# Optimization experiments

Measured on AMD Instinct MI355X. Metric: run time of the kernel, lower is better.

Reference implementation:

```python
import jax, jax.numpy as jnp
import numpy as np

LSTM_H = 128
HID = 64
EMB = 64
GRU2_H = 50
B, T = 2048, 200
NODE_NUM = 50000


def _lstm_dir(x_proj, w_hh, reverse):
    # x_proj: (T, B, 4H) = x @ W_ih^T + b_ih + b_hh, precomputed
    Bn = x_proj.shape[1]
    H = w_hh.shape[1]
    h0 = jnp.zeros((Bn, H), x_proj.dtype)

    def step(carry, xp):
        h, c = carry
        gates = xp + h @ w_hh.T
        i, f, g, o = jnp.split(gates, 4, axis=-1)  # torch gate order i,f,g,o
        i = jax.nn.sigmoid(i); f = jax.nn.sigmoid(f)
        g = jnp.tanh(g); o = jax.nn.sigmoid(o)
        c = f * c + i * g
        h = o * jnp.tanh(c)
        return (h, c), h

    (hT, _), hs = jax.lax.scan(step, (h0, h0), x_proj, reverse=reverse)
    return hs, hT  # hs: (T,B,H) time-aligned; hT: final hidden of this direction


def _bilstm(x, wih_f, whh_f, b_f, wih_b, whh_b, b_b):
    # x: (B,T,I) batch_first -> scan over time
    xt = jnp.swapaxes(x, 0, 1)  # (T,B,I)
    hs_f, h_f = _lstm_dir(xt @ wih_f.T + b_f, whh_f, False)
    hs_b, h_b = _lstm_dir(xt @ wih_b.T + b_b, whh_b, True)
    out = jnp.concatenate([hs_f, hs_b], axis=-1)  # (T,B,2H)
    return jnp.swapaxes(out, 0, 1), jnp.stack([h_f, h_b])  # (B,T,2H), (2,B,H)


def _gru(x, h, wih, whh, bih, bhh):
    gi = x @ wih.T + bih
    gh = h @ whh.T + bhh
    ir, iz, inn = jnp.split(gi, 3, axis=-1)  # torch gate order r,z,n
    hr, hz, hn = jnp.split(gh, 3, axis=-1)
    r = jax.nn.sigmoid(ir + hr)
    z = jax.nn.sigmoid(iz + hz)
    n = jnp.tanh(inn + r * hn)
    return (1.0 - z) * n + z * h


def setup_inputs() -> dict:
    key = jax.random.key(0)
    ks = iter(jax.random.split(key, 40))
    s = 0.05
    d = {}
    d['node_data'] = jax.random.randint(next(ks), (B, 2), 0, NODE_NUM)
    d['edge_data'] = jax.random.uniform(next(ks), (B, T, 1), jnp.float32)
    d['emb'] = jax.random.normal(next(ks), (NODE_NUM, EMB), jnp.float32) * s
    # LSTM 1: input 1, hidden 128, bidirectional (b = b_ih + b_hh fused)
    d['l1_wih_f'] = jax.random.normal(next(ks), (4 * LSTM_H, 1), jnp.float32) * s
    d['l1_whh_f'] = jax.random.normal(next(ks), (4 * LSTM_H, LSTM_H), jnp.float32) * s
    d['l1_b_f'] = jax.random.normal(next(ks), (4 * LSTM_H,), jnp.float32) * s
    d['l1_wih_b'] = jax.random.normal(next(ks), (4 * LSTM_H, 1), jnp.float32) * s
    d['l1_whh_b'] = jax.random.normal(next(ks), (4 * LSTM_H, LSTM_H), jnp.float32) * s
    d['l1_b_b'] = jax.random.normal(next(ks), (4 * LSTM_H,), jnp.float32) * s
    # LSTM 2: input 256, hidden 128, bidirectional
    d['l2_wih_f'] = jax.random.normal(next(ks), (4 * LSTM_H, 2 * LSTM_H), jnp.float32) * s
    d['l2_whh_f'] = jax.random.normal(next(ks), (4 * LSTM_H, LSTM_H), jnp.float32) * s
    d['l2_b_f'] = jax.random.normal(next(ks), (4 * LSTM_H,), jnp.float32) * s
    d['l2_wih_b'] = jax.random.normal(next(ks), (4 * LSTM_H, 2 * LSTM_H), jnp.float32) * s
    d['l2_whh_b'] = jax.random.normal(next(ks), (4 * LSTM_H, LSTM_H), jnp.float32) * s
    d['l2_b_b'] = jax.random.normal(next(ks), (4 * LSTM_H,), jnp.float32) * s
    # encoder FCs
    d['fc1_w'] = jax.random.normal(next(ks), (2 * LSTM_H, 2 * LSTM_H), jnp.float32) * s
    d['fc1_b'] = jnp.zeros((2 * LSTM_H,), jnp.float32)
    d['fc2_w'] = jax.random.normal(next(ks), (HID, 2 * LSTM_H), jnp.float32) * s
    d['fc2_b'] = jnp.zeros((HID,), jnp.float32)
    # GRUCell 1: input 1, hidden HID+EMB=128
    G1 = HID + EMB
    d['g1_wih'] = jax.random.normal(next(ks), (3 * G1, 1), jnp.float32) * s
    d['g1_whh'] = jax.random.normal(next(ks), (3 * G1, G1), jnp.float32) * s
    d['g1_bih'] = jax.random.normal(next(ks), (3 * G1,), jnp.float32) * s
    d['g1_bhh'] = jax.random.normal(next(ks), (3 * G1,), jnp.float32) * s
    # GRUCell 2: input 128, hidden 50
    d['g2_wih'] = jax.random.normal(next(ks), (3 * GRU2_H, G1), jnp.float32) * s
    d['g2_whh'] = jax.random.normal(next(ks), (3 * GRU2_H, GRU2_H), jnp.float32) * s
    d['g2_bih'] = jax.random.normal(next(ks), (3 * GRU2_H,), jnp.float32) * s
    d['g2_bhh'] = jax.random.normal(next(ks), (3 * GRU2_H,), jnp.float32) * s
    # decoder FC: 50 -> 1
    d['dec_w'] = jax.random.normal(next(ks), (1, GRU2_H), jnp.float32) * s
    d['dec_b'] = jnp.zeros((1,), jnp.float32)
    return d


def reference(node_data, edge_data, emb,
              l1_wih_f, l1_whh_f, l1_b_f, l1_wih_b, l1_whh_b, l1_b_b,
              l2_wih_f, l2_whh_f, l2_b_f, l2_wih_b, l2_whh_b, l2_b_b,
              fc1_w, fc1_b, fc2_w, fc2_b,
              g1_wih, g1_whh, g1_bih, g1_bhh,
              g2_wih, g2_whh, g2_bih, g2_bhh,
              dec_w, dec_b):
    # ---- encoder ----
    node_embs = emb[node_data]                      # (B,2,EMB)
    node_emb = node_embs.mean(axis=1)               # (head+tail)/2
    h1_out, hn1 = _bilstm(edge_data, l1_wih_f, l1_whh_f, l1_b_f,
                          l1_wih_b, l1_whh_b, l1_b_b)
    _, hn2 = _bilstm(h1_out, l2_wih_f, l2_whh_f, l2_b_f,
                     l2_wih_b, l2_whh_b, l2_b_b)
    # faithful to original: view (2,B,128) -> (-1, 256) row-major (interleaves dir/batch)
    hidden_lstm = hn1.reshape(-1, 2 * LSTM_H) + hn2.reshape(-1, 2 * LSTM_H)
    h_fc1 = jax.nn.sigmoid(hidden_lstm @ fc1_w.T + fc1_b)  # dropout = identity (eval)
    temp_emb = jax.nn.sigmoid(h_fc1 @ fc2_w.T + fc2_b)
    hidden = jnp.concatenate([temp_emb, node_emb], axis=1)  # (B, HID+EMB)
    # ---- decoder: sequential GRU unroll as a scan ----
    Bn, max_len = edge_data.shape[0], edge_data.shape[1]
    h2_0 = jnp.zeros((Bn, GRU2_H), edge_data.dtype)

    def dstep(carry, _):
        res, h1, h2 = carry
        h1n = _gru(res, h1, g1_wih, g1_whh, g1_bih, g1_bhh)
        h2n = _gru(h1n, h2, g2_wih, g2_whh, g2_bih, g2_bhh)
        resn = jax.nn.sigmoid(h2n @ dec_w.T + dec_b)        # (B,1)
        return (resn, h1n, h2n), resn

    init = (edge_data[:, -1], hidden, h2_0)
    _, results = jax.lax.scan(dstep, init, None, length=max_len)
    return jnp.swapaxes(results, 0, 1)  # (B, max_len, 1)
```

## Files before the change

### kernel.cpp

```cpp
#include <hip/hip_runtime.h>
#include <stdint.h>

typedef short bf16x8 __attribute__((ext_vector_type(8)));
typedef float f32x4  __attribute__((ext_vector_type(4)));
typedef unsigned short u16;

#define NBATCH 2048
#define NT 200

#define MFMA_AG(accv, av, wfrag) \
  asm("v_mfma_f32_16x16x32_bf16 %0, %1, %2, %0" : "+v"(accv) : "v"(av), "a"(wfrag))
#define SEED_A(x) asm volatile("" : "+a"(x))

#define OFF_HN1   209715200ull
#define OFF_HN2   211812352ull
#define OFF_ZC    213909504ull

__device__ __forceinline__ short f2bf(float f){
  union { float f; uint32_t u; } v; v.f = f;
  uint32_t u = v.u;
  u += 0x7fffu + ((u >> 16) & 1u);
  return (short)(u >> 16);
}
__device__ __forceinline__ float sigm(float x){
  return __builtin_amdgcn_rcpf(1.0f + __expf(-x));
}
__device__ __forceinline__ float tanh_(float x){
  return fmaf(-2.0f, __builtin_amdgcn_rcpf(1.0f + __expf(2.0f * x)), 1.0f);
}

__global__ void prep_l12(const float* __restrict__ l1hf, const float* __restrict__ l1hb,
                         const float* __restrict__ l2wf, const float* __restrict__ l2hf,
                         const float* __restrict__ l2wb, const float* __restrict__ l2hb,
                         u16* __restrict__ wl1, u16* __restrict__ wl2)
{
  int idx = blockIdx.x * 256 + threadIdx.x;
  if (idx < 16384){
    int tid = idx & 511, r = idx >> 9;
    int kt = r & 3, g = (r >> 2) & 3, d = r >> 4;
    const float* whh = d ? l1hb : l1hf;
    int wv = tid >> 6, ln = tid & 63, lr = ln & 15, lk = ln >> 4;
    int n = g * 128 + wv * 16 + lr;
    const float* s = whh + (size_t)n * 128 + kt * 32 + lk * 8;
    bf16x8 w;
#pragma unroll
    for (int i = 0; i < 8; ++i) w[i] = f2bf(s[i]);
    *(bf16x8*)(wl1 + (size_t)idx * 8) = w;
  } else {
    int j = idx - 16384;
    int tid = j & 511, r = j >> 9;
    int kt = r % 12, rg = r / 12;
    int g = rg & 3, d = rg >> 2;
    const float* wih = d ? l2wb : l2wf;
    const float* whh = d ? l2hb : l2hf;
    int wv = tid >> 6, ln = tid & 63, lr = ln & 15, lk = ln >> 4;
    int n = g * 128 + wv * 16 + lr;
    const float* s = (kt < 8) ? (wih + (size_t)n * 256 + kt * 32 + lk * 8)
                              : (whh + (size_t)n * 128 + (kt - 8) * 32 + lk * 8);
    bf16x8 w;
#pragma unroll
    for (int i = 0; i < 8; ++i) w[i] = f2bf(s[i]);
    *(bf16x8*)(wl2 + (size_t)j * 8) = w;
  }
}

__global__ void prep_dec(const float* __restrict__ g1whh, const float* __restrict__ g2wih,
                         const float* __restrict__ g2whh,
                         u16* __restrict__ wd1, u16* __restrict__ wd2i, u16* __restrict__ wd2h)
{
  int idx = blockIdx.x * 256 + threadIdx.x;
  if (idx < 6144){
    int tid = idx & 511, r = idx >> 9;
    int kt = r & 3, g = r >> 2;
    int wv = tid >> 6, ln = tid & 63, lr = ln & 15, lk = ln >> 4;
    int n = g * 128 + wv * 16 + lr;
    const float* s = g1whh + (size_t)n * 128 + kt * 32 + lk * 8;
    bf16x8 w;
#pragma unroll
    for (int i = 0; i < 8; ++i) w[i] = f2bf(s[i]);
    *(bf16x8*)(wd1 + (size_t)idx * 8) = w;
  } else if (idx < 9216){
    int j = idx - 6144;
    int tid = j & 255, r = j >> 8;
    int kt = r & 3, g = r >> 2;
    int wv = tid >> 6, ln = tid & 63, lr = ln & 15, lk = ln >> 4;
    int jj = wv * 16 + lr;
    bf16x8 w;
#pragma unroll
    for (int i = 0; i < 8; ++i){
      int k = kt * 32 + lk * 8 + i;
      w[i] = (jj < 50) ? f2bf(g2wih[(size_t)(g * 50 + jj) * 128 + k]) : (short)0;
    }
    *(bf16x8*)(wd2i + (size_t)j * 8) = w;
  } else {
    int j = idx - 9216;
    int tid = j & 255, r = j >> 8;
    int kt = r & 1, g = r >> 1;
    int wv = tid >> 6, ln = tid & 63, lr = ln & 15, lk = ln >> 4;
    int jj = wv * 16 + lr;
    bf16x8 w;
#pragma unroll
    for (int i = 0; i < 8; ++i){
      int k = kt * 32 + lk * 8 + i;
      w[i] = (jj < 50 && k < 50) ? f2bf(g2whh[(size_t)(g * 50 + jj) * 50 + k]) : (short)0;
    }
    *(bf16x8*)(wd2h + (size_t)j * 8) = w;
  }
}

__global__ void prep_fcT(const float* __restrict__ fc1w, const float* __restrict__ fc2w,
                         float* __restrict__ fc1wT, float* __restrict__ fc2wT)
{
  int idx = blockIdx.x * 256 + threadIdx.x;
  if (idx < 65536){
    int n = idx & 255, k = idx >> 8;
    fc1wT[(size_t)k * 256 + n] = fc1w[(size_t)n * 256 + k];
  } else {
    int j = idx - 65536;
    int m = j & 63, k = j >> 6;
    fc2wT[(size_t)k * 64 + m] = fc2w[(size_t)m * 256 + k];
  }
}

__global__ void k_node(const int* __restrict__ nd, const float* __restrict__ emb,
                       float* __restrict__ ne){
  int t = blockIdx.x * 256 + threadIdx.x;
  if (t >= NBATCH * 64) return;
  int row = t >> 6, e = t & 63;
  int i0 = nd[row * 2], i1 = nd[row * 2 + 1];
  ne[t] = 0.5f * (emb[(size_t)i0 * 64 + e] + emb[(size_t)i1 * 64 + e]);
}

__global__ __launch_bounds__(512) __attribute__((amdgpu_waves_per_eu(2, 2))) void k_l1(
    const float* __restrict__ edge, const u16* __restrict__ wl1,
    const float* __restrict__ wih_f, const float* __restrict__ b_f,
    const float* __restrict__ wih_b, const float* __restrict__ b_b,
    u16* __restrict__ h1out, float* __restrict__ hn1)
{
  const int bid = blockIdx.x;
  const int dir = bid >> 7;
  const int b0  = (bid & 127) * 16;
  const float* wih = dir ? wih_b : wih_f;
  const float* bia = dir ? b_b  : b_f;

  const int tid = threadIdx.x;
  const int wv  = tid >> 6;
  const int ln  = tid & 63;
  const int lr  = ln & 15;
  const int lk  = ln >> 4;

  __shared__ __align__(16) short hbf[2][16 * 128];
  __shared__ float xall[16][NT];

  bf16x8 W[4][4];
  const u16* wb = wl1 + (size_t)dir * 16 * 512 * 8;
  float wv_[4], bv_[4];
#pragma unroll
  for (int g = 0; g < 4; ++g){
    int n = g * 128 + wv * 16 + lr;
    wv_[g] = wih[n];
    bv_[g] = bia[n];
#pragma unroll
    for (int kt = 0; kt < 4; ++kt){
      W[g][kt] = *(const bf16x8*)(wb + ((size_t)(g * 4 + kt) * 512 + tid) * 8);
      SEED_A(W[g][kt]);
    }
  }
  for (int i = tid; i < 16 * 128; i += 512) hbf[0][i] = 0;
  for (int i = tid; i < 16 * NT; i += 512){
    int r = i / NT, t = i - r * NT;
    xall[r][t] = edge[(b0 + r) * NT + t];
  }
  float cst[4] = {0.f, 0.f, 0.f, 0.f};
  float hseg[4] = {0.f, 0.f, 0.f, 0.f};
  __syncthreads();

  for (int s = 0; s < NT; ++s){
    const int p = s & 1;
    const int t = dir ? (NT - 1 - s) : s;

    const char* hb = (const char*)hbf + p * (16 * 256);
    f32x4 acc[4];
    float xq[4];
#pragma unroll
    for (int q = 0; q < 4; ++q) xq[q] = xall[lk * 4 + q][t];
#pragma unroll
    for (int g = 0; g < 4; ++g){
#pragma unroll
      for (int q = 0; q < 4; ++q) acc[g][q] = fmaf(xq[q], wv_[g], bv_[g]);
    }
#pragma unroll
    for (int kt = 0; kt < 4; ++kt){
      int off = lr * 256 + ((kt * 64 + lk * 16) ^ ((lr & 7) << 4));
      bf16x8 a = *(const bf16x8*)(hb + off);
#pragma unroll
      for (int g = 0; g < 4; ++g) MFMA_AG(acc[g], a, W[g][kt]);
    }
    char* hbw = (char*)hbf + (p ^ 1) * (16 * 256);
#pragma unroll
    for (int q = 0; q < 4; ++q){
      float iv = sigm(acc[0][q]);
      float fv = sigm(acc[1][q]);
      float gv = tanh_(acc[2][q]);
      float ov = sigm(acc[3][q]);
      cst[q] = fv * cst[q] + iv * gv;
      hseg[q] = ov * tanh_(cst[q]);
      short hv = f2bf(hseg[q]);
      int r = lk * 4 + q, j = wv * 16 + lr;
      h1out[((size_t)t * NBATCH + b0 + r) * 256 + dir * 128 + j] = (u16)hv;
      *(short*)(hbw + r * 256 + ((2 * j) ^ ((r & 7) << 4))) = hv;
    }
    __syncthreads();
  }
#pragma unroll
  for (int q = 0; q < 4; ++q)
    hn1[((size_t)dir * NBATCH + b0 + lk * 4 + q) * 128 + wv * 16 + lr] = hseg[q];
}

__global__ __launch_bounds__(512) __attribute__((amdgpu_waves_per_eu(2, 2))) void k_l2(
    const u16* __restrict__ h1out, const u16* __restrict__ wl2,
    const float* __restrict__ b_f, const float* __restrict__ b_b,
    float* __restrict__ hn2)
{
  const int bid = blockIdx.x;
  const int dir = bid >> 7;
  const int b0  = (bid & 127) * 16;
  const float* bia = dir ? b_b : b_f;

  const int tid = threadIdx.x;
  const int wv  = tid >> 6;
  const int ln  = tid & 63;
  const int lr  = ln & 15;
  const int lk  = ln >> 4;

  __shared__ __align__(16) short wlds[16 * 512 * 8];
  __shared__ __align__(16) short Ab[2][16 * 384];

  const u16* wb = wl2 + (size_t)dir * 48 * 512 * 8;
#pragma unroll
  for (int f = 0; f < 16; ++f){
    int g = f >> 2, kt = f & 3;
    *(bf16x8*)&wlds[((size_t)f * 512 + tid) * 8] =
        *(const bf16x8*)(wb + ((size_t)(g * 12 + kt) * 512 + tid) * 8);
  }
  bf16x8 Wa[4][8];
  float bv_[4];
#pragma unroll
  for (int g = 0; g < 4; ++g){
    bv_[g] = bia[g * 128 + wv * 16 + lr];
#pragma unroll
    for (int k8 = 0; k8 < 8; ++k8){
      Wa[g][k8] = *(const bf16x8*)(wb + ((size_t)(g * 12 + 4 + k8) * 512 + tid) * 8);
      SEED_A(Wa[g][k8]);
    }
  }
  for (int i = tid; i < 16 * 128; i += 512){
    int r = i >> 7, j = i & 127;
    *(short*)((char*)Ab + r * 768 + ((512 + 2 * j) ^ ((r & 7) << 4))) = 0;
  }
  const int sr = tid >> 5, sg = tid & 31;
  {
    int t0 = dir ? NT - 1 : 0;
    bf16x8 v = *(const bf16x8*)(h1out + ((size_t)t0 * NBATCH + b0 + sr) * 256 + sg * 8);
    *(bf16x8*)((char*)Ab + sr * 768 + ((sg * 16) ^ ((sr & 7) << 4))) = v;
  }
  float cst[4] = {0.f, 0.f, 0.f, 0.f};
  float hseg[4] = {0.f, 0.f, 0.f, 0.f};
  __syncthreads();

  for (int s = 0; s < NT; ++s){
    const int p = s & 1;
    const int t = dir ? (NT - 1 - s) : s;
    const int tn = dir ? (t > 0 ? t - 1 : 0) : (t < NT - 1 ? t + 1 : NT - 1);
    bf16x8 xr = *(const bf16x8*)(h1out + ((size_t)tn * NBATCH + b0 + sr) * 256 + sg * 8);

    const char* ab = (const char*)Ab + p * (16 * 768);
    f32x4 acc[4];
#pragma unroll
    for (int g = 0; g < 4; ++g){
#pragma unroll
      for (int q = 0; q < 4; ++q) acc[g][q] = bv_[g];
    }
#pragma unroll
    for (int kt = 0; kt < 4; ++kt){
      int off = lr * 768 + ((kt * 64 + lk * 16) ^ ((lr & 7) << 4));
      bf16x8 a = *(const bf16x8*)(ab + off);
#pragma unroll
      for (int g = 0; g < 4; ++g){
        bf16x8 w = *(const bf16x8*)&wlds[((size_t)(g * 4 + kt) * 512 + tid) * 8];
        acc[g] = __builtin_amdgcn_mfma_f32_16x16x32_bf16(a, w, acc[g], 0, 0, 0);
      }
    }
#pragma unroll
    for (int k8 = 0; k8 < 8; ++k8){
      int kt = 4 + k8;
      int off = lr * 768 + ((kt * 64 + lk * 16) ^ ((lr & 7) << 4));
      bf16x8 a = *(const bf16x8*)(ab + off);
#pragma unroll
      for (int g = 0; g < 4; ++g) MFMA_AG(acc[g], a, Wa[g][k8]);
    }
    char* abw = (char*)Ab + (p ^ 1) * (16 * 768);
#pragma unroll
    for (int q = 0; q < 4; ++q){
      float iv = sigm(acc[0][q]);
      float fv = sigm(acc[1][q]);
      float gv = tanh_(acc[2][q]);
      float ov = sigm(acc[3][q]);
      cst[q] = fv * cst[q] + iv * gv;
      hseg[q] = ov * tanh_(cst[q]);
      int r = lk * 4 + q, j = wv * 16 + lr;
      *(short*)(abw + r * 768 + ((512 + 2 * j) ^ ((r & 7) << 4))) = f2bf(hseg[q]);
    }
    *(bf16x8*)(abw + sr * 768 + ((sg * 16) ^ ((sr & 7) << 4))) = xr;
    __syncthreads();
  }
#pragma unroll
  for (int q = 0; q < 4; ++q)
    hn2[((size_t)dir * NBATCH + b0 + lk * 4 + q) * 128 + wv * 16 + lr] = hseg[q];
}

__global__ __launch_bounds__(256) void k_fc(
    const float* __restrict__ hn1, const float* __restrict__ hn2,
    const float* __restrict__ fc1wT, const float* __restrict__ fc1b,
    const float* __restrict__ fc2wT, const float* __restrict__ fc2b,
    const float* __restrict__ ne, float* __restrict__ hidden)
{
  __shared__ float X[16][256];
  __shared__ float Y[16][256];
  const int b0 = blockIdx.x * 16;
  const int tid = threadIdx.x;
  for (int i = tid; i < 16 * 256; i += 256){
    int rr = i >> 8, cc = i & 255;
    size_t o = (size_t)(b0 + rr) * 256 + cc;
    X[rr][cc] = hn1[o] + hn2[o];
  }
  __syncthreads();
  {
    const int n = tid;
    float a[16];
#pragma unroll
    for (int r = 0; r < 16; ++r) a[r] = fc1b[n];
    for (int k = 0; k < 256; ++k){
      float w = fc1wT[(size_t)k * 256 + n];
#pragma unroll
      for (int r = 0; r < 16; ++r) a[r] = fmaf(X[r][k], w, a[r]);
    }
#pragma unroll
    for (int r = 0; r < 16; ++r) Y[r][n] = sigm(a[r]);
  }
  __syncthreads();
  {
    const int m = tid & 63, rg = tid >> 6;
    float a2[4];
#pragma unroll
    for (int q = 0; q < 4; ++q) a2[q] = fc2b[m];
    for (int k = 0; k < 256; ++k){
      float w = fc2wT[(size_t)k * 64 + m];
#pragma unroll
      for (int q = 0; q < 4; ++q) a2[q] = fmaf(Y[rg * 4 + q][k], w, a2[q]);
    }
#pragma unroll
    for (int q = 0; q < 4; ++q)
      hidden[(size_t)(b0 + rg * 4 + q) * 128 + m] = sigm(a2[q]);
  }
  for (int i = tid; i < 16 * 64; i += 256){
    int rr = i >> 6, e = i & 63;
    hidden[(size_t)(b0 + rr) * 128 + 64 + e] = ne[(size_t)(b0 + rr) * 64 + e];
  }
}

__global__ __launch_bounds__(512) __attribute__((amdgpu_waves_per_eu(2, 2))) void k_dec(
    const float* __restrict__ edge, const float* __restrict__ hidden,
    const float* __restrict__ g1wih, const float* __restrict__ g1bih,
    const float* __restrict__ g1bhh, const u16* __restrict__ wd1,
    const float* __restrict__ g2bih, const float* __restrict__ g2bhh,
    const u16* __restrict__ wd2i, const u16* __restrict__ wd2h,
    const float* __restrict__ decw, const float* __restrict__ decb,
    float* __restrict__ out)
{
  const int b0 = blockIdx.x * 16;
  const int tid = threadIdx.x;
  const int wv  = tid >> 6;
  const int ln  = tid & 63;
  const int lr  = ln & 15;
  const int lk  = ln >> 4;

  __shared__ __align__(16) short h1bf[2][16 * 128];
  __shared__ __align__(16) short h2bf[2][16 * 64];
  __shared__ float part[2][4][16];

  bf16x8 W1[3][4];
  float wih1v[3], bih1v[3], bhh1v[3];
#pragma unroll
  for (int g = 0; g < 3; ++g){
    int n = g * 128 + wv * 16 + lr;
    wih1v[g] = g1wih[n];
    bih1v[g] = g1bih[n];
    bhh1v[g] = g1bhh[n];
#pragma unroll
    for (int kt = 0; kt < 4; ++kt){
      W1[g][kt] = *(const bf16x8*)(wd1 + ((size_t)(g * 4 + kt) * 512 + tid) * 8);
      SEED_A(W1[g][kt]);
    }
  }
  bf16x8 Wi2[3][4], Wh2[3][2];
  float bih2v[3] = {0,0,0}, bhh2v[3] = {0,0,0}, dwv = 0.f;
  const int jj = wv * 16 + lr;
  if (wv < 4){
    bool nv_ = (jj < 50);
    dwv = nv_ ? decw[jj] : 0.f;
#pragma unroll
    for (int g = 0; g < 3; ++g){
      bih2v[g] = nv_ ? g2bih[g * 50 + jj] : 0.f;
      bhh2v[g] = nv_ ? g2bhh[g * 50 + jj] : 0.f;
#pragma unroll
      for (int kt = 0; kt < 4; ++kt){
        Wi2[g][kt] = *(const bf16x8*)(wd2i + ((size_t)(g * 4 + kt) * 256 + tid) * 8);
        SEED_A(Wi2[g][kt]);
      }
#pragma unroll
      for (int kt = 0; kt < 2; ++kt){
        Wh2[g][kt] = *(const bf16x8*)(wd2h + ((size_t)(g * 2 + kt) * 256 + tid) * 8);
        SEED_A(Wh2[g][kt]);
      }
    }
  }
  float h1s[4], h2s[4] = {0.f, 0.f, 0.f, 0.f}, e4[4];
#pragma unroll
  for (int q = 0; q < 4; ++q){
    h1s[q] = hidden[(size_t)(b0 + lk * 4 + q) * 128 + wv * 16 + lr];
    int r = lk * 4 + q, j = wv * 16 + lr;
    *(short*)((char*)h1bf + r * 256 + ((2 * j) ^ ((r & 7) << 4))) = f2bf(h1s[q]);
    e4[q] = edge[(b0 + r) * NT + NT - 1];
  }
  for (int i = tid; i < 16 * 64; i += 512) h2bf[0][i] = 0;
  const float db = decb[0];
  __syncthreads();

  for (int s = 0; s < NT; ++s){
    const int p = s & 1;
    float res_q[4];
    if (s == 0){
#pragma unroll
      for (int q = 0; q < 4; ++q) res_q[q] = e4[q];
    } else {
#pragma unroll
      for (int q = 0; q < 4; ++q){
        int row = lk * 4 + q;
        float sum = part[p][0][row] + part[p][1][row] + part[p][2][row] + part[p][3][row] + db;
        res_q[q] = sigm(sum);
        if (wv == 0 && lr == 0) out[(size_t)(b0 + row) * NT + (s - 1)] = res_q[q];
      }
    }
    const char* h1r = (const char*)h1bf + p * (16 * 256);
    f32x4 ar, az, an;
#pragma unroll
    for (int q = 0; q < 4; ++q){ ar[q] = bhh1v[0]; az[q] = bhh1v[1]; an[q] = bhh1v[2]; }
#pragma unroll
    for (int kt = 0; kt < 4; ++kt){
      int off = lr * 256 + ((kt * 64 + lk * 16) ^ ((lr & 7) << 4));
      bf16x8 a = *(const bf16x8*)(h1r + off);
      MFMA_AG(ar, a, W1[0][kt]);
      MFMA_AG(az, a, W1[1][kt]);
      MFMA_AG(an, a, W1[2][kt]);
    }
    char* h1w = (char*)h1bf + (p ^ 1) * (16 * 256);
#pragma unroll
    for (int q = 0; q < 4; ++q){
      float res = res_q[q];
      float rv = sigm(fmaf(res, wih1v[0], bih1v[0]) + ar[q]);
      float zv = sigm(fmaf(res, wih1v[1], bih1v[1]) + az[q]);
      float nv = tanh_(fmaf(res, wih1v[2], bih1v[2]) + rv * an[q]);
      h1s[q] = (1.f - zv) * nv + zv * h1s[q];
      int r = lk * 4 + q, j = wv * 16 + lr;
      *(short*)(h1w + r * 256 + ((2 * j) ^ ((r & 7) << 4))) = f2bf(h1s[q]);
    }
    __syncthreads();
    if (wv < 4){
      f32x4 gi0, gi1, gi2v, gh0, gh1, gh2v;
#pragma unroll
      for (int q = 0; q < 4; ++q){
        gi0[q] = bih2v[0]; gi1[q] = bih2v[1]; gi2v[q] = bih2v[2];
        gh0[q] = bhh2v[0]; gh1[q] = bhh2v[1]; gh2v[q] = bhh2v[2];
      }
      const char* h1n = (const char*)h1bf + (p ^ 1) * (16 * 256);
#pragma unroll
      for (int kt = 0; kt < 4; ++kt){
        int off = lr * 256 + ((kt * 64 + lk * 16) ^ ((lr & 7) << 4));
        bf16x8 a = *(const bf16x8*)(h1n + off);
        MFMA_AG(gi0,  a, Wi2[0][kt]);
        MFMA_AG(gi1,  a, Wi2[1][kt]);
        MFMA_AG(gi2v, a, Wi2[2][kt]);
      }
      const char* h2r = (const char*)h2bf + p * (16 * 128);
#pragma unroll
      for (int kt = 0; kt < 2; ++kt){
        int off = lr * 128 + ((kt * 64 + lk * 16) ^ ((lr & 7) << 4));
        bf16x8 a = *(const bf16x8*)(h2r + off);
        MFMA_AG(gh0,  a, Wh2[0][kt]);
        MFMA_AG(gh1,  a, Wh2[1][kt]);
        MFMA_AG(gh2v, a, Wh2[2][kt]);
      }
      char* h2w = (char*)h2bf + (p ^ 1) * (16 * 128);
      float pd[4];
#pragma unroll
      for (int q = 0; q < 4; ++q){
        float r2 = sigm(gi0[q] + gh0[q]);
        float z2 = sigm(gi1[q] + gh1[q]);
        float n2 = tanh_(gi2v[q] + r2 * gh2v[q]);
        h2s[q] = (1.f - z2) * n2 + z2 * h2s[q];
        pd[q] = h2s[q] * dwv;
        int r = lk * 4 + q, j = wv * 16 + lr;
        *(short*)(h2w + r * 128 + ((2 * j) ^ ((r & 7) << 4))) = f2bf(h2s[q]);
      }
#pragma unroll
      for (int m = 1; m < 16; m <<= 1){
#pragma unroll
        for (int q = 0; q < 4; ++q) pd[q] += __shfl_xor(pd[q], m);
      }
      if (lr == 0){
#pragma unroll
        for (int q = 0; q < 4; ++q) part[p ^ 1][wv][lk * 4 + q] = pd[q];
      }
    }
    __syncthreads();
  }
  if (wv == 0 && lr == 0){
#pragma unroll
    for (int q = 0; q < 4; ++q){
      int row = lk * 4 + q;
      float sum = part[0][0][row] + part[0][1][row] + part[0][2][row] + part[0][3][row] + db;
      out[(size_t)(b0 + row) * NT + (NT - 1)] = sigm(sum);
    }
  }
}

extern "C" void kernel_launch(void* const* d_in, const int* in_sizes, int n_in,
                              void* d_out, int out_size, void* d_ws, size_t ws_size,
                              hipStream_t stream)
{
  (void)in_sizes; (void)n_in; (void)out_size; (void)ws_size;
  const int*   nd    = (const int*)  d_in[0];
  const float* edge  = (const float*)d_in[1];
  const float* emb   = (const float*)d_in[2];
  const float* l1wf  = (const float*)d_in[3];
  const float* l1hf  = (const float*)d_in[4];
  const float* l1bf  = (const float*)d_in[5];
  const float* l1wb  = (const float*)d_in[6];
  const float* l1hb  = (const float*)d_in[7];
  const float* l1bb  = (const float*)d_in[8];
  const float* l2wf  = (const float*)d_in[9];
  const float* l2hf  = (const float*)d_in[10];
  const float* l2bf  = (const float*)d_in[11];
  const float* l2wb  = (const float*)d_in[12];
  const float* l2hb  = (const float*)d_in[13];
  const float* l2bb  = (const float*)d_in[14];
  const float* fc1w  = (const float*)d_in[15];
  const float* fc1b  = (const float*)d_in[16];
  const float* fc2w  = (const float*)d_in[17];
  const float* fc2b  = (const float*)d_in[18];
  const float* g1wih = (const float*)d_in[19];
  const float* g1whh = (const float*)d_in[20];
  const float* g1bih = (const float*)d_in[21];
  const float* g1bhh = (const float*)d_in[22];
  const float* g2wih = (const float*)d_in[23];
  const float* g2whh = (const float*)d_in[24];
  const float* g2bih = (const float*)d_in[25];
  const float* g2bhh = (const float*)d_in[26];
  const float* decw  = (const float*)d_in[27];
  const float* decb  = (const float*)d_in[28];

  char* ws = (char*)d_ws;
  u16*   h1out  = (u16*)ws;
  u16*   wd1    = (u16*)ws;
  u16*   wd2i   = (u16*)(ws + 98304);
  u16*   wd2h   = (u16*)(ws + 147456);
  float* fc1wT  = (float*)(ws + 262144);
  float* fc2wT  = (float*)(ws + 524288);
  float* hn1    = (float*)(ws + OFF_HN1);
  float* hn2    = (float*)(ws + OFF_HN2);
  u16*   wl2    = (u16*)(ws + OFF_ZC);
  u16*   wl1    = (u16*)(ws + OFF_ZC + 786432);
  float* ne     = (float*)(ws + OFF_ZC);
  float* hidden = (float*)(ws + OFF_ZC + 524288);

  prep_l12<<<dim3(256), dim3(256), 0, stream>>>(l1hf, l1hb, l2wf, l2hf, l2wb, l2hb, wl1, wl2);
  k_l1<<<dim3(256), dim3(512), 0, stream>>>(edge, wl1, l1wf, l1bf, l1wb, l1bb, h1out, hn1);
  k_l2<<<dim3(256), dim3(512), 0, stream>>>(h1out, wl2, l2bf, l2bb, hn2);
  prep_dec<<<dim3(42), dim3(256), 0, stream>>>(g1whh, g2wih, g2whh, wd1, wd2i, wd2h);
  prep_fcT<<<dim3(320), dim3(256), 0, stream>>>(fc1w, fc2w, fc1wT, fc2wT);
  k_node<<<dim3(512), dim3(256), 0, stream>>>(nd, emb, ne);
  k_fc<<<dim3(128), dim3(256), 0, stream>>>(hn1, hn2, fc1wT, fc1b, fc2wT, fc2b, ne, hidden);
  k_dec<<<dim3(128), dim3(512), 0, stream>>>(edge, hidden, g1wih, g1bih, g1bhh, wd1,
                                             g2bih, g2bhh, wd2i, wd2h, decw, decb,
                                             (float*)d_out);
}
```

Baseline: 1.057 ms.

## Merge small prep kernels, stagger MFMA k-order per wave, use lighter barriers

```diff
diff --git a/kernel.cpp b/kernel.cpp
--- a/kernel.cpp
+++ b/kernel.cpp
@@ -11,6 +11,7 @@
 #define MFMA_AG(accv, av, wfrag) \
   asm("v_mfma_f32_16x16x32_bf16 %0, %1, %2, %0" : "+v"(accv) : "v"(av), "a"(wfrag))
 #define SEED_A(x) asm volatile("" : "+a"(x))
+#define BAR() asm volatile("s_waitcnt lgkmcnt(0)\n\ts_barrier" ::: "memory")
 
 #define OFF_HN1   209715200ull
 #define OFF_HN2   211812352ull
@@ -64,9 +65,13 @@
   }
 }
 
-__global__ void prep_dec(const float* __restrict__ g1whh, const float* __restrict__ g2wih,
-                         const float* __restrict__ g2whh,
-                         u16* __restrict__ wd1, u16* __restrict__ wd2i, u16* __restrict__ wd2h)
+__global__ void prep2(const float* __restrict__ g1whh, const float* __restrict__ g2wih,
+                      const float* __restrict__ g2whh,
+                      const float* __restrict__ fc1w, const float* __restrict__ fc2w,
+                      const int* __restrict__ nd, const float* __restrict__ emb,
+                      u16* __restrict__ wd1, u16* __restrict__ wd2i, u16* __restrict__ wd2h,
+                      float* __restrict__ fc1wT, float* __restrict__ fc2wT,
+                      float* __restrict__ ne)
 {
   int idx = blockIdx.x * 256 + threadIdx.x;
   if (idx < 6144){
@@ -92,7 +97,7 @@
       w[i] = (jj < 50) ? f2bf(g2wih[(size_t)(g * 50 + jj) * 128 + k]) : (short)0;
     }
     *(bf16x8*)(wd2i + (size_t)j * 8) = w;
-  } else {
+  } else if (idx < 10752){
     int j = idx - 9216;
     int tid = j & 255, r = j >> 8;
     int kt = r & 1, g = r >> 1;
@@ -105,31 +110,27 @@
       w[i] = (jj < 50 && k < 50) ? f2bf(g2whh[(size_t)(g * 50 + jj) * 50 + k]) : (short)0;
     }
     *(bf16x8*)(wd2h + (size_t)j * 8) = w;
-  }
-}
-
-__global__ void prep_fcT(const float* __restrict__ fc1w, const float* __restrict__ fc2w,
-                         float* __restrict__ fc1wT, float* __restrict__ fc2wT)
-{
-  int idx = blockIdx.x * 256 + threadIdx.x;
-  if (idx < 65536){
-    int n = idx & 255, k = idx >> 8;
+  } else if (idx < 10752 + 65536){
+    int j = idx - 10752;
+    int n = j & 255, k = j >> 8;
     fc1wT[(size_t)k * 256 + n] = fc1w[(size_t)n * 256 + k];
-  } else {
-    int j = idx - 65536;
+  } else if (idx < 10752 + 81920){
+    int j = idx - 10752 - 65536;
     int m = j & 63, k = j >> 6;
     fc2wT[(size_t)k * 64 + m] = fc2w[(size_t)m * 256 + k];
-  }
-}
-
-__global__ void k_node(const int* __restrict__ nd, const float* __restrict__ emb,
-                       float* __restrict__ ne){
-  int t = blockIdx.x * 256 + threadIdx.x;
-  if (t >= NBATCH * 64) return;
-  int row = t >> 6, e = t & 63;
-  int i0 = nd[row * 2], i1 = nd[row * 2 + 1];
-  ne[t] = 0.5f * (emb[(size_t)i0 * 64 + e] + emb[(size_t)i1 * 64 + e]);
-}
+  } else {
+    int t = idx - 92672;
+    int row = t >> 6, e = t & 63;
+    int i0 = nd[row * 2], i1 = nd[row * 2 + 1];
+    ne[t] = 0.5f * (emb[(size_t)i0 * 64 + e] + emb[(size_t)i1 * 64 + e]);
+  }
+}
+
+#define L1_KT(kt) { \
+  int off = lr * 256 + (((kt) * 64 + lk * 16) ^ ((lr & 7) << 4)); \
+  bf16x8 a = *(const bf16x8*)(hb + off); \
+  MFMA_AG(acc[0], a, W[0][kt]); MFMA_AG(acc[1], a, W[1][kt]); \
+  MFMA_AG(acc[2], a, W[2][kt]); MFMA_AG(acc[3], a, W[3][kt]); }
 
 __global__ __launch_bounds__(512) __attribute__((amdgpu_waves_per_eu(2, 2))) void k_l1(
     const float* __restrict__ edge, const u16* __restrict__ wl1,
@@ -189,13 +190,8 @@
 #pragma unroll
       for (int q = 0; q < 4; ++q) acc[g][q] = fmaf(xq[q], wv_[g], bv_[g]);
     }
-#pragma unroll
-    for (int kt = 0; kt < 4; ++kt){
-      int off = lr * 256 + ((kt * 64 + lk * 16) ^ ((lr & 7) << 4));
-      bf16x8 a = *(const bf16x8*)(hb + off);
-#pragma unroll
-      for (int g = 0; g < 4; ++g) MFMA_AG(acc[g], a, W[g][kt]);
-    }
+    if (wv & 1){ L1_KT(2) L1_KT(3) L1_KT(0) L1_KT(1) }
+    else       { L1_KT(0) L1_KT(1) L1_KT(2) L1_KT(3) }
     char* hbw = (char*)hbf + (p ^ 1) * (16 * 256);
 #pragma unroll
     for (int q = 0; q < 4; ++q){
@@ -210,12 +206,30 @@
       h1out[((size_t)t * NBATCH + b0 + r) * 256 + dir * 128 + j] = (u16)hv;
       *(short*)(hbw + r * 256 + ((2 * j) ^ ((r & 7) << 4))) = hv;
     }
-    __syncthreads();
+    BAR();
   }
 #pragma unroll
   for (int q = 0; q < 4; ++q)
     hn1[((size_t)dir * NBATCH + b0 + lk * 4 + q) * 128 + wv * 16 + lr] = hseg[q];
 }
+
+#define L2_LDSKT(kt) { \
+  int off = lr * 768 + (((kt) * 64 + lk * 16) ^ ((lr & 7) << 4)); \
+  bf16x8 a = *(const bf16x8*)(ab + off); \
+  bf16x8 w0 = *(const bf16x8*)&wlds[((size_t)(0 * 4 + (kt)) * 512 + tid) * 8]; \
+  acc[0] = __builtin_amdgcn_mfma_f32_16x16x32_bf16(a, w0, acc[0], 0, 0, 0); \
+  bf16x8 w1 = *(const bf16x8*)&wlds[((size_t)(1 * 4 + (kt)) * 512 + tid) * 8]; \
+  acc[1] = __builtin_amdgcn_mfma_f32_16x16x32_bf16(a, w1, acc[1], 0, 0, 0); \
+  bf16x8 w2 = *(const bf16x8*)&wlds[((size_t)(2 * 4 + (kt)) * 512 + tid) * 8]; \
+  acc[2] = __builtin_amdgcn_mfma_f32_16x16x32_bf16(a, w2, acc[2], 0, 0, 0); \
+  bf16x8 w3 = *(const bf16x8*)&wlds[((size_t)(3 * 4 + (kt)) * 512 + tid) * 8]; \
+  acc[3] = __builtin_amdgcn_mfma_f32_16x16x32_bf16(a, w3, acc[3], 0, 0, 0); }
+
+#define L2_AGKT(k8) { \
+  int off = lr * 768 + (((4 + (k8)) * 64 + lk * 16) ^ ((lr & 7) << 4)); \
+  bf16x8 a = *(const bf16x8*)(ab + off); \
+  MFMA_AG(acc[0], a, Wa[0][k8]); MFMA_AG(acc[1], a, Wa[1][k8]); \
+  MFMA_AG(acc[2], a, Wa[2][k8]); MFMA_AG(acc[3], a, Wa[3][k8]); }
 
 __global__ __launch_bounds__(512) __attribute__((amdgpu_waves_per_eu(2, 2))) void k_l2(
     const u16* __restrict__ h1out, const u16* __restrict__ wl2,
@@ -281,23 +295,14 @@
 #pragma unroll
       for (int q = 0; q < 4; ++q) acc[g][q] = bv_[g];
     }
-#pragma unroll
-    for (int kt = 0; kt < 4; ++kt){
-      int off = lr * 768 + ((kt * 64 + lk * 16) ^ ((lr & 7) << 4));
-      bf16x8 a = *(const bf16x8*)(ab + off);
-#pragma unroll
-      for (int g = 0; g < 4; ++g){
-        bf16x8 w = *(const bf16x8*)&wlds[((size_t)(g * 4 + kt) * 512 + tid) * 8];
-        acc[g] = __builtin_amdgcn_mfma_f32_16x16x32_bf16(a, w, acc[g], 0, 0, 0);
-      }
-    }
-#pragma unroll
-    for (int k8 = 0; k8 < 8; ++k8){
-      int kt = 4 + k8;
-      int off = lr * 768 + ((kt * 64 + lk * 16) ^ ((lr & 7) << 4));
-      bf16x8 a = *(const bf16x8*)(ab + off);
-#pragma unroll
-      for (int g = 0; g < 4; ++g) MFMA_AG(acc[g], a, Wa[g][k8]);
+    if (wv & 1){
+      L2_AGKT(0) L2_AGKT(1) L2_AGKT(2) L2_AGKT(3)
+      L2_AGKT(4) L2_AGKT(5) L2_AGKT(6) L2_AGKT(7)
+      L2_LDSKT(0) L2_LDSKT(1) L2_LDSKT(2) L2_LDSKT(3)
+    } else {
+      L2_LDSKT(0) L2_LDSKT(1) L2_LDSKT(2) L2_LDSKT(3)
+      L2_AGKT(0) L2_AGKT(1) L2_AGKT(2) L2_AGKT(3)
+      L2_AGKT(4) L2_AGKT(5) L2_AGKT(6) L2_AGKT(7)
     }
     char* abw = (char*)Ab + (p ^ 1) * (16 * 768);
 #pragma unroll
@@ -312,7 +317,7 @@
       *(short*)(abw + r * 768 + ((512 + 2 * j) ^ ((r & 7) << 4))) = f2bf(hseg[q]);
     }
     *(bf16x8*)(abw + sr * 768 + ((sg * 16) ^ ((sr & 7) << 4))) = xr;
-    __syncthreads();
+    BAR();
   }
 #pragma unroll
   for (int q = 0; q < 4; ++q)
@@ -369,6 +374,16 @@
   }
 }
 
+#define D1_KT(kt) { \
+  int off = lr * 256 + (((kt) * 64 + lk * 16) ^ ((lr & 7) << 4)); \
+  bf16x8 a = *(const bf16x8*)(h1r + off); \
+  MFMA_AG(ar, a, W1[0][kt]); MFMA_AG(az, a, W1[1][kt]); MFMA_AG(an, a, W1[2][kt]); }
+
+#define D2_KT(kt) { \
+  int off = lr * 256 + (((kt) * 64 + lk * 16) ^ ((lr & 7) << 4)); \
+  bf16x8 a = *(const bf16x8*)(h1n + off); \
+  MFMA_AG(gi0, a, Wi2[0][kt]); MFMA_AG(gi1, a, Wi2[1][kt]); MFMA_AG(gi2v, a, Wi2[2][kt]); }
+
 __global__ __launch_bounds__(512) __attribute__((amdgpu_waves_per_eu(2, 2))) void k_dec(
     const float* __restrict__ edge, const float* __restrict__ hidden,
     const float* __restrict__ g1wih, const float* __restrict__ g1bih,
@@ -456,14 +471,8 @@
     f32x4 ar, az, an;
 #pragma unroll
     for (int q = 0; q < 4; ++q){ ar[q] = bhh1v[0]; az[q] = bhh1v[1]; an[q] = bhh1v[2]; }
-#pragma unroll
-    for (int kt = 0; kt < 4; ++kt){
-      int off = lr * 256 + ((kt * 64 + lk * 16) ^ ((lr & 7) << 4));
-      bf16x8 a = *(const bf16x8*)(h1r + off);
-      MFMA_AG(ar, a, W1[0][kt]);
-      MFMA_AG(az, a, W1[1][kt]);
-      MFMA_AG(an, a, W1[2][kt]);
-    }
+    if (wv & 1){ D1_KT(2) D1_KT(3) D1_KT(0) D1_KT(1) }
+    else       { D1_KT(0) D1_KT(1) D1_KT(2) D1_KT(3) }
     char* h1w = (char*)h1bf + (p ^ 1) * (16 * 256);
 #pragma unroll
     for (int q = 0; q < 4; ++q){
@@ -475,7 +484,7 @@
       int r = lk * 4 + q, j = wv * 16 + lr;
       *(short*)(h1w + r * 256 + ((2 * j) ^ ((r & 7) << 4))) = f2bf(h1s[q]);
     }
-    __syncthreads();
+    BAR();
     if (wv < 4){
       f32x4 gi0, gi1, gi2v, gh0, gh1, gh2v;
 #pragma unroll
@@ -484,14 +493,8 @@
         gh0[q] = bhh2v[0]; gh1[q] = bhh2v[1]; gh2v[q] = bhh2v[2];
       }
       const char* h1n = (const char*)h1bf + (p ^ 1) * (16 * 256);
-#pragma unroll
-      for (int kt = 0; kt < 4; ++kt){
-        int off = lr * 256 + ((kt * 64 + lk * 16) ^ ((lr & 7) << 4));
-        bf16x8 a = *(const bf16x8*)(h1n + off);
-        MFMA_AG(gi0,  a, Wi2[0][kt]);
-        MFMA_AG(gi1,  a, Wi2[1][kt]);
-        MFMA_AG(gi2v, a, Wi2[2][kt]);
-      }
+      if (wv & 1){ D2_KT(2) D2_KT(3) D2_KT(0) D2_KT(1) }
+      else       { D2_KT(0) D2_KT(1) D2_KT(2) D2_KT(3) }
       const char* h2r = (const char*)h2bf + p * (16 * 128);
 #pragma unroll
       for (int kt = 0; kt < 2; ++kt){
@@ -523,7 +526,7 @@
         for (int q = 0; q < 4; ++q) part[p ^ 1][wv][lk * 4 + q] = pd[q];
       }
     }
-    __syncthreads();
+    BAR();
   }
   if (wv == 0 && lr == 0){
 #pragma unroll
@@ -587,9 +590,8 @@
   prep_l12<<<dim3(256), dim3(256), 0, stream>>>(l1hf, l1hb, l2wf, l2hf, l2wb, l2hb, wl1, wl2);
   k_l1<<<dim3(256), dim3(512), 0, stream>>>(edge, wl1, l1wf, l1bf, l1wb, l1bb, h1out, hn1);
   k_l2<<<dim3(256), dim3(512), 0, stream>>>(h1out, wl2, l2bf, l2bb, hn2);
-  prep_dec<<<dim3(42), dim3(256), 0, stream>>>(g1whh, g2wih, g2whh, wd1, wd2i, wd2h);
-  prep_fcT<<<dim3(320), dim3(256), 0, stream>>>(fc1w, fc2w, fc1wT, fc2wT);
-  k_node<<<dim3(512), dim3(256), 0, stream>>>(nd, emb, ne);
+  prep2<<<dim3(874), dim3(256), 0, stream>>>(g1whh, g2wih, g2whh, fc1w, fc2w, nd, emb,
+                                             wd1, wd2i, wd2h, fc1wT, fc2wT, ne);
   k_fc<<<dim3(128), dim3(256), 0, stream>>>(hn1, hn2, fc1wT, fc1b, fc2wT, fc2b, ne, hidden);
   k_dec<<<dim3(128), dim3(512), 0, stream>>>(edge, hidden, g1wih, g1bih, g1bhh, wd1,
                                              g2bih, g2bhh, wd2i, wd2h, decw, decb,
```

After: 1.046 ms. About the same (-1.0%).
